# Optimization experiments

Hardware: AMD Instinct MI355X
Metric: run time of the kernel (lower is better)

## Reference

```python
import jax, jax.numpy as jnp
import numpy as np

N = 100000      # nodes
E = 1600000     # edges
P = 262144      # pos/neg candidate edges
IN = 128        # in_channels
HID = 64        # hidden_channels
HEADS = 2
NEG_SLOPE = 0.2  # PyG GATConv default


def setup_inputs() -> dict:
    key = jax.random.key(0)
    ks = jax.random.split(key, 16)
    g = lambda k, shape, fan_in: jax.random.normal(k, shape, jnp.float32) * (1.0 / np.sqrt(fan_in))
    return {
        "x": jax.random.normal(ks[0], (N, IN), jnp.float32),
        "edge_index": jax.random.randint(ks[1], (2, E), 0, N),
        "edge_weight": jax.random.uniform(ks[2], (E,), jnp.float32),
        "pos_edge_index": jax.random.randint(ks[3], (2, P), 0, N),
        "neg_edge_index": jax.random.randint(ks[4], (2, P), 0, N),
        # conv1: in -> HEADS*HID
        "W1": g(ks[5], (IN, HEADS * HID), IN),
        "att_src1": g(ks[6], (HEADS, HID), HID),
        "att_dst1": g(ks[7], (HEADS, HID), HID),
        "b1": jnp.zeros((HEADS * HID,), jnp.float32),
        # conv2: HEADS*HID -> HID (heads=1)
        "W2": g(ks[8], (HEADS * HID, HID), HEADS * HID),
        "att_src2": g(ks[9], (1, HID), HID),
        "att_dst2": g(ks[10], (1, HID), HID),
        "b2": jnp.zeros((HID,), jnp.float32),
        # link_pred: Linear(2*HID, 1)
        "link_W": g(ks[11], (2 * HID, 1), 2 * HID),
        "link_b": jnp.zeros((1,), jnp.float32),
    }


def gat_layer(x, src, dst, W, a_src, a_dst, bias, heads, out_c, concat):
    n = x.shape[0]
    xw = (x @ W).reshape(n, heads, out_c)                      # [N, H, C]
    alpha_src = jnp.sum(xw * a_src, axis=-1)                   # [N, H]
    alpha_dst = jnp.sum(xw * a_dst, axis=-1)                   # [N, H]
    e = jax.nn.leaky_relu(alpha_src[src] + alpha_dst[dst], NEG_SLOPE)  # [E, H]
    # segment softmax over edges grouped by destination node
    m = jax.ops.segment_max(e, dst, num_segments=n)            # [N, H]
    ex = jnp.exp(e - m[dst])
    s = jax.ops.segment_sum(ex, dst, num_segments=n)
    alpha = ex / s[dst]                                        # [E, H]
    out = jax.ops.segment_sum(xw[src] * alpha[..., None], dst, num_segments=n)  # [N, H, C]
    out = out.reshape(n, heads * out_c) if concat else out.mean(axis=1)
    return out + bias


def reference(x, edge_index, edge_weight, pos_edge_index, neg_edge_index,
              W1, att_src1, att_dst1, b1, W2, att_src2, att_dst2, b2,
              link_W, link_b):
    n = x.shape[0]
    # PyG GATConv add_self_loops=True
    loop = jnp.arange(n)
    src = jnp.concatenate([edge_index[0], loop])
    dst = jnp.concatenate([edge_index[1], loop])

    h = gat_layer(x, src, dst, W1, att_src1, att_dst1, b1, HEADS, HID, True)
    h = jax.nn.relu(h)
    z = gat_layer(h, src, dst, W2, att_src2, att_dst2, b2, 1, HID, True)

    def decode(ei):
        feat = jnp.concatenate([z[ei[0]], z[ei[1]]], axis=1)   # [P, 2*HID]
        return (feat @ link_W + link_b).squeeze(-1)

    return decode(pos_edge_index), decode(neg_edge_index)
```

## Files before the change

kernel.cpp:

```cpp
#include <hip/hip_runtime.h>

#define N_NODES 100000
#define E_EDGES 1600000
#define EP      (E_EDGES + N_NODES)
#define P_CAND  262144
#define IN_C    128
#define HID     64
#define NEG_SLOPE 0.2f

#define NBIN  196
#define NB2   256
#define EPB   ((EP + NB2 - 1) / NB2)
#define NTOT  (NBIN * NB2)

typedef _Float16 half4v __attribute__((ext_vector_type(4)));
typedef _Float16 half8v __attribute__((ext_vector_type(8)));
typedef float    float4v __attribute__((ext_vector_type(4)));


__global__ __launch_bounds__(256) void hist_kernel(const int* __restrict__ ei,
                                                   int* __restrict__ hist) {
    __shared__ int lh[NBIN];
    for (int t = threadIdx.x; t < NBIN; t += 256) lh[t] = 0;
    __syncthreads();
    int start = blockIdx.x * EPB;
    int end = min(start + EPB, EP);
    for (int i = start + threadIdx.x; i < end; i += 256) {
        int dst = (i < E_EDGES) ? ei[E_EDGES + i] : (i - E_EDGES);
        atomicAdd(&lh[dst >> 9], 1);
    }
    __syncthreads();
    for (int t = threadIdx.x; t < NBIN; t += 256) hist[t * NB2 + blockIdx.x] = lh[t];
}

__global__ __launch_bounds__(256) void scanA_kernel(const int* __restrict__ hist,
                                                    int* __restrict__ rowscan,
                                                    int* __restrict__ binsum) {
    int t = blockIdx.x;
    int c = threadIdx.x;
    int v = hist[t * NB2 + c];
    int lane = c & 63, w = c >> 6;
    int iv = v;
#pragma unroll
    for (int d = 1; d < 64; d <<= 1) {
        int o = __shfl_up(iv, d);
        if (lane >= d) iv += o;
    }
    __shared__ int wt[4];
    if (lane == 63) wt[w] = iv;
    __syncthreads();
    int add = 0;
    for (int i = 0; i < w; i++) add += wt[i];
    int inc = iv + add;
    rowscan[t * NB2 + c] = inc - v;
    if (c == 255) binsum[t] = inc;
}

__global__ __launch_bounds__(256) void scanB_kernel(const int* __restrict__ binsum,
                                                    int* __restrict__ binoff) {
    __shared__ int s[256];
    int c = threadIdx.x;
    int v = (c < NBIN) ? binsum[c] : 0;
    s[c] = v;
    __syncthreads();
    for (int d = 1; d < 256; d <<= 1) {
        int o = (c >= d) ? s[c - d] : 0;
        __syncthreads();
        s[c] += o;
        __syncthreads();
    }
    if (c == 0) binoff[0] = 0;
    if (c < NBIN) binoff[c + 1] = s[c];
}

__global__ __launch_bounds__(256) void scatterbin_kernel(const int* __restrict__ ei,
                                                         const int* __restrict__ rowscan,
                                                         const int* __restrict__ binoff,
                                                         unsigned* __restrict__ binned) {
    __shared__ int cur[NBIN];
    for (int t = threadIdx.x; t < NBIN; t += 256)
        cur[t] = binoff[t] + rowscan[t * NB2 + blockIdx.x];
    __syncthreads();
    int start = blockIdx.x * EPB;
    int end = min(start + EPB, EP);
    for (int i = start + threadIdx.x; i < end; i += 256) {
        int src, dst;
        if (i < E_EDGES) { src = ei[i]; dst = ei[E_EDGES + i]; }
        else             { src = i - E_EDGES; dst = src; }
        int pos = atomicAdd(&cur[dst >> 9], 1);
        binned[pos] = (unsigned)src | ((unsigned)(dst & 511) << 17);
    }
}

__global__ __launch_bounds__(1024) void binsort_kernel(const unsigned* __restrict__ binned,
                                                       const int* __restrict__ binoff,
                                                       int* __restrict__ off,
                                                       int* __restrict__ csr) {
    __shared__ int lh[512];
    __shared__ int wpre[8];
    int b = blockIdx.x, t = threadIdx.x;
    int base = binoff[b];
    int endv = binoff[b + 1];
    if (t < 512) lh[t] = 0;
    __syncthreads();
    for (int i = base + t; i < endv; i += 1024)
        atomicAdd(&lh[binned[i] >> 17], 1);
    __syncthreads();
    int iv = 0, lane = t & 63, w = t >> 6;
    if (t < 512) {
        iv = lh[t];
#pragma unroll
        for (int d = 1; d < 64; d <<= 1) {
            int o = __shfl_up(iv, d);
            if (lane >= d) iv += o;
        }
        if (lane == 63) wpre[w] = iv;
    }
    __syncthreads();
    if (t == 0) {
        int run = 0;
        for (int i = 0; i < 8; i++) { int x = wpre[i]; wpre[i] = run; run += x; }
    }
    __syncthreads();
    if (t < 512) {
        int ex = iv + wpre[w] - lh[t];
        int node = b * 512 + t;
        if (node <= N_NODES) off[node] = base + ex;
        lh[t] = base + ex;
    }
    __syncthreads();
    for (int i = base + t; i < endv; i += 1024) {
        unsigned v = binned[i];
        int pos = atomicAdd(&lh[v >> 17], 1);
        csr[pos] = (int)(v & 0x1FFFFu);
    }
}


__global__ __launch_bounds__(256) void prep_kernel(
        const float* __restrict__ W1, const float* __restrict__ W2,
        const float* __restrict__ att_src1, const float* __restrict__ att_dst1,
        const float* __restrict__ att_src2, const float* __restrict__ att_dst2,
        const float* __restrict__ b2, const float* __restrict__ lw,
        _Float16* __restrict__ W1T, _Float16* __restrict__ W2T,
        float* __restrict__ cvec) {
    int idx = blockIdx.x * 256 + threadIdx.x;
    if (idx < 16384) {
        int col = idx >> 7, k = idx & 127;
        W1T[idx] = (_Float16)W1[k * 128 + col];
    } else if (idx < 16896) {
        int j = idx - 16384;
        int c4 = j >> 7, k = j & 127;
        const float* av = (c4 < 2 ? att_src1 : att_dst1) + (c4 & 1) * 64;
        const float* wr = W1 + k * 128 + (c4 & 1) * 64;
        float s = 0.f;
        for (int c = 0; c < 64; c++) s += wr[c] * av[c];
        W1T[(128 + c4) * 128 + k] = (_Float16)s;
    } else if (idx < 18432) {
        W1T[132 * 128 + (idx - 16896)] = (_Float16)0.f;
    } else if (idx < 18944) {
        int j = idx - 18432;
        int c4 = j >> 7, k = j & 127;
        const float* av = (c4 == 0) ? att_src2 : (c4 == 1) ? att_dst2
                        : (c4 == 2) ? lw : (lw + 64);
        const float* wr = W2 + k * 64;
        float s = 0.f;
        for (int c = 0; c < 64; c++) s += wr[c] * av[c];
        W2T[c4 * 128 + k] = (_Float16)s;
    } else if (idx < 18946) {
        int c = idx - 18944;
        const float* lwp = lw + c * 64;
        float s = 0.f;
        for (int i = 0; i < 64; i++) s += b2[i] * lwp[i];
        cvec[c] = s;
    }
}


__global__ __launch_bounds__(256) void gemm1_kernel(
        const float* __restrict__ x, const _Float16* __restrict__ W1T,
        unsigned char* __restrict__ xw1q, float* __restrict__ asp1,
        float* __restrict__ ad1) {
    __shared__ _Float16 xs[64 * 136];
    int tid = threadIdx.x;
    int base = blockIdx.x * 64;
    int w = tid >> 6, l = tid & 63;
    int quad = l >> 4, lq = l & 15;
    int row = base + 16 * w + lq;
    size_t rb = (size_t)(row < N_NODES ? row : 0) * 32;
    const float4* x4 = (const float4*)x;
    float4 af[8];
#pragma unroll
    for (int ks = 0; ks < 4; ks++) {
        af[2 * ks]     = x4[rb + ks * 8 + quad * 2];
        af[2 * ks + 1] = x4[rb + ks * 8 + quad * 2 + 1];
    }
    half8v a[4];
#pragma unroll
    for (int ks = 0; ks < 4; ks++) {
        float4 u0 = af[2 * ks], u1 = af[2 * ks + 1];
        half8v t;
        t[0] = (_Float16)u0.x; t[1] = (_Float16)u0.y; t[2] = (_Float16)u0.z; t[3] = (_Float16)u0.w;
        t[4] = (_Float16)u1.x; t[5] = (_Float16)u1.y; t[6] = (_Float16)u1.z; t[7] = (_Float16)u1.w;
        a[ks] = t;
    }
    float4v acc[9];
#pragma unroll
    for (int t = 0; t < 9; t++) acc[t] = (float4v)0.f;
#pragma unroll
    for (int ks = 0; ks < 4; ++ks) {
#pragma unroll
        for (int t = 0; t < 9; t++) {
            half8v b = *(const half8v*)&W1T[(t * 16 + lq) * 128 + ks * 32 + quad * 8];
            acc[t] = __builtin_amdgcn_mfma_f32_16x16x32_f16(a[ks], b, acc[t], 0, 0, 0);
        }
    }
    if (lq < 4) {
#pragma unroll
        for (int r = 0; r < 4; r++) {
            int n = base + 16 * w + quad * 4 + r;
            if (n < N_NODES) {
                if (lq < 2) asp1[4 * n + lq] = acc[8][r];
                else        ad1[2 * n + (lq & 1)] = acc[8][r];
            }
        }
    }
#pragma unroll
    for (int t = 0; t < 8; t++)
#pragma unroll
        for (int r = 0; r < 4; r++)
            xs[(16 * w + quad * 4 + r) * 136 + t * 16 + lq] = (_Float16)acc[t][r];
    __syncthreads();
    int node = tid >> 2, seg = tid & 3;
    if (base + node < N_NODES) {
        float vals[32];
        float mx = 0.f;
#pragma unroll
        for (int i = 0; i < 4; i++) {
            half8v vv = *(const half8v*)&xs[node * 136 + seg * 32 + i * 8];
#pragma unroll
            for (int k = 0; k < 8; k++) {
                float f = (float)vv[k];
                vals[i * 8 + k] = f;
                mx = fmaxf(mx, fabsf(f));
            }
        }
        mx = fmaxf(mx, __shfl_xor(mx, 1));
        mx = fmaxf(mx, __shfl_xor(mx, 2));
        mx = fmaxf(mx, 1e-20f);
        float r = 127.f / mx;
        unsigned pk[8];
#pragma unroll
        for (int d = 0; d < 8; d++) {
            unsigned u0 = (unsigned)(__float2int_rn(vals[d * 4 + 0] * r) + 128);
            unsigned u1 = (unsigned)(__float2int_rn(vals[d * 4 + 1] * r) + 128);
            unsigned u2 = (unsigned)(__float2int_rn(vals[d * 4 + 2] * r) + 128);
            unsigned u3 = (unsigned)(__float2int_rn(vals[d * 4 + 3] * r) + 128);
            pk[d] = u0 | (u1 << 8) | (u2 << 16) | (u3 << 24);
        }
        unsigned* dst = (unsigned*)&xw1q[(size_t)(base + node) * 128 + seg * 32];
        *(uint4*)dst       = make_uint4(pk[0], pk[1], pk[2], pk[3]);
        *(uint4*)(dst + 4) = make_uint4(pk[4], pk[5], pk[6], pk[7]);
        if (seg == 0) asp1[4 * (base + node) + 2] = mx * (1.f / 127.f);
    }
}


__global__ __launch_bounds__(256) void agg1_kernel(
        const int* __restrict__ off, const int* __restrict__ csr_src,
        const float* __restrict__ asp1, const float* __restrict__ ad1,
        const unsigned char* __restrict__ xw1q, const float* __restrict__ b1,
        const _Float16* __restrict__ W2T, float* __restrict__ asp2) {
    __shared__ float2 esm[4][64];
    int wv = threadIdx.x >> 6, lane = threadIdx.x & 63;
    int ql = lane & 15;
    int gb = lane & 48;
    int n = blockIdx.x * 16 + (wv << 2) + (lane >> 4);
    int s = off[n], e = off[n + 1];
    float2 ad = *(const float2*)&ad1[2 * n];
    float adn0 = ad.x, adn1 = ad.y;
    const char* fl = (const char*)&esm[wv][gb] + ((ql >= 8) ? 4 : 0);
    const unsigned char* xq = xw1q + 8 * ql;
    float acc[8];
#pragma unroll
    for (int i = 0; i < 8; i++) acc[i] = 0.f;
    float sl0 = 0.f, sl1 = 0.f;
    float csum = 0.f;

#define DEQ1(QV, G) { \
    acc[0] = fmaf((float)((QV).x & 0xffu), (G), acc[0]); \
    acc[1] = fmaf((float)(((QV).x >> 8) & 0xffu), (G), acc[1]); \
    acc[2] = fmaf((float)(((QV).x >> 16) & 0xffu), (G), acc[2]); \
    acc[3] = fmaf((float)((QV).x >> 24), (G), acc[3]); \
    acc[4] = fmaf((float)((QV).y & 0xffu), (G), acc[4]); \
    acc[5] = fmaf((float)(((QV).y >> 8) & 0xffu), (G), acc[5]); \
    acc[6] = fmaf((float)(((QV).y >> 16) & 0xffu), (G), acc[6]); \
    acc[7] = fmaf((float)((QV).y >> 24), (G), acc[7]); }

    for (int b = s; b < e; b += 16) {
        int cnt = min(16, e - b);
        int l = ql < cnt ? ql : cnt - 1;
        int srcv = csr_src[b + l];
        float4 ap = *(const float4*)&asp1[4 * srcv];
        float e0 = ap.x + adn0; e0 = e0 > 0.f ? e0 : NEG_SLOPE * e0;
        float e1 = ap.y + adn1; e1 = e1 > 0.f ? e1 : NEG_SLOPE * e1;
        float f0v = (ql < cnt) ? __expf(e0) : 0.f;
        float f1v = (ql < cnt) ? __expf(e1) : 0.f;
        sl0 += f0v; sl1 += f1v;
        esm[wv][lane] = make_float2(f0v * ap.z, f1v * ap.z);
        int sj = __shfl(srcv, gb);
        uint2 qcur = *(const uint2*)&xq[(size_t)sj * 128];
        int j = 0;
        for (; j + 1 < cnt; ++j) {
            int sn = __shfl(srcv, gb + j + 1);
            uint2 qnxt = *(const uint2*)&xq[(size_t)sn * 128];
            float g = *(const float*)(fl + (size_t)j * 8);
            csum += g;
            DEQ1(qcur, g)
            qcur = qnxt;
        }
        { float g = *(const float*)(fl + (size_t)j * 8);
          csum += g; DEQ1(qcur, g) }
    }
#undef DEQ1
#pragma unroll
    for (int m = 8; m >= 1; m >>= 1) { sl0 += __shfl_xor(sl0, m); sl1 += __shfl_xor(sl1, m); }
    float sum = (ql >= 8) ? sl1 : sl0;
    float rs = __builtin_amdgcn_rcpf(sum);
    float base8 = -128.f * csum;
    int c = 8 * ql;
    float z[8];
#pragma unroll
    for (int i = 0; i < 8; i++) {
        float vv = fmaf(acc[i] + base8, rs, b1[c + i]);
        z[i] = vv > 0.f ? vv : 0.f;
    }
    half8v w0 = *(const half8v*)&W2T[0 * 128 + c];
    half8v w1 = *(const half8v*)&W2T[1 * 128 + c];
    half8v w2 = *(const half8v*)&W2T[2 * 128 + c];
    half8v w3 = *(const half8v*)&W2T[3 * 128 + c];
    float d0 = 0.f, d1 = 0.f, d2 = 0.f, d3 = 0.f;
#pragma unroll
    for (int i = 0; i < 8; i++) {
        d0 = fmaf(z[i], (float)w0[i], d0);
        d1 = fmaf(z[i], (float)w1[i], d1);
        d2 = fmaf(z[i], (float)w2[i], d2);
        d3 = fmaf(z[i], (float)w3[i], d3);
    }
#pragma unroll
    for (int m = 8; m >= 1; m >>= 1) {
        d0 += __shfl_xor(d0, m);
        d1 += __shfl_xor(d1, m);
        d2 += __shfl_xor(d2, m);
        d3 += __shfl_xor(d3, m);
    }
    if (ql == 0) {
        *(float4*)&asp2[4 * n] = make_float4(d0, d2, d3, d1);
    }
}


__global__ __launch_bounds__(256) void agg2_kernel(
        const int* __restrict__ off, const int* __restrict__ csr_src,
        const float* __restrict__ asp2, const float* __restrict__ cvec,
        float* __restrict__ u, float* __restrict__ v) {
    int wv = threadIdx.x >> 6, lane = threadIdx.x & 63;
    int ql = lane & 15;
    int n = blockIdx.x * 16 + (wv << 2) + (lane >> 4);
    int s = off[n], e = off[n + 1];
    float adn = asp2[4 * n + 3];
    float sf = 0.f, s1 = 0.f, s2 = 0.f;
    for (int j = s + ql; j < e; j += 16) {
        int srcv = csr_src[j];
        float4 ap = *(const float4*)&asp2[4 * srcv];
        float ev = ap.x + adn; ev = ev > 0.f ? ev : NEG_SLOPE * ev;
        float f = __expf(ev);
        sf += f;
        s1 = fmaf(f, ap.y, s1);
        s2 = fmaf(f, ap.z, s2);
    }
#pragma unroll
    for (int m = 8; m >= 1; m >>= 1) {
        sf += __shfl_xor(sf, m);
        s1 += __shfl_xor(s1, m);
        s2 += __shfl_xor(s2, m);
    }
    if (ql == 0) {
        float rs = __builtin_amdgcn_rcpf(sf);
        u[n] = fmaf(s1, rs, cvec[0]);
        v[n] = fmaf(s2, rs, cvec[1]);
    }
}


__global__ __launch_bounds__(256) void decode_kernel(
        const int* __restrict__ pos_ei, const int* __restrict__ neg_ei,
        const float* __restrict__ u, const float* __restrict__ v,
        const float* __restrict__ lb, float* __restrict__ out) {
    int idx = blockIdx.x * 256 + threadIdx.x;
    if (idx >= 2 * P_CAND) return;
    const int* ei; int p;
    if (idx < P_CAND) { ei = pos_ei; p = idx; }
    else              { ei = neg_ei; p = idx - P_CAND; }
    int sN = ei[p], dN = ei[P_CAND + p];
    out[idx] = u[sN] + v[dN] + lb[0];
}


extern "C" void kernel_launch(void* const* d_in, const int* in_sizes, int n_in,
                              void* d_out, int out_size, void* d_ws, size_t ws_size,
                              hipStream_t stream) {
    const float* x        = (const float*)d_in[0];
    const int*   ei       = (const int*)d_in[1];
    const int*   pos_ei   = (const int*)d_in[3];
    const int*   neg_ei   = (const int*)d_in[4];
    const float* W1       = (const float*)d_in[5];
    const float* att_src1 = (const float*)d_in[6];
    const float* att_dst1 = (const float*)d_in[7];
    const float* b1       = (const float*)d_in[8];
    const float* W2       = (const float*)d_in[9];
    const float* att_src2 = (const float*)d_in[10];
    const float* att_dst2 = (const float*)d_in[11];
    const float* b2       = (const float*)d_in[12];
    const float* lw       = (const float*)d_in[13];
    const float* lb       = (const float*)d_in[14];
    float* out = (float*)d_out;

    char* ws = (char*)d_ws;
    size_t o = 0;
    auto alloc = [&](size_t bytes) -> char* {
        char* p = ws + o;
        o += (bytes + 511) & ~(size_t)511;
        return p;
    };
    unsigned char* xw1q = (unsigned char*)alloc((size_t)N_NODES * 128);
    float*    asp1  = (float*)alloc((size_t)N_NODES * 4 * 4);
    float*    ad1   = (float*)alloc((size_t)N_NODES * 2 * 4);
    float*    asp2  = (float*)alloc((size_t)N_NODES * 4 * 4);
    float*    cvec  = (float*)alloc(512);
    float*    u     = (float*)alloc((size_t)N_NODES * 4);
    float*    v     = (float*)alloc((size_t)N_NODES * 4);
    int*      off   = (int*)alloc((size_t)(N_NODES + 1) * 4);
    int*      hist  = (int*)alloc((size_t)NTOT * 4);
    int*      rowscan = (int*)alloc((size_t)NTOT * 4);
    int*      binsum  = (int*)alloc(256 * 4);
    int*      binoff  = (int*)alloc(256 * 4);
    unsigned* binned= (unsigned*)alloc((size_t)EP * 4);
    int*      csr   = (int*)alloc((size_t)EP * 4);
    _Float16* W1T   = (_Float16*)alloc((size_t)144 * 128 * 2);
    _Float16* W2T   = (_Float16*)alloc((size_t)4 * 128 * 2);

    prep_kernel<<<75, 256, 0, stream>>>(W1, W2, att_src1, att_dst1, att_src2, att_dst2,
                                        b2, lw, W1T, W2T, cvec);
    hist_kernel<<<NB2, 256, 0, stream>>>(ei, hist);
    scanA_kernel<<<NBIN, 256, 0, stream>>>(hist, rowscan, binsum);
    scanB_kernel<<<1, 256, 0, stream>>>(binsum, binoff);
    scatterbin_kernel<<<NB2, 256, 0, stream>>>(ei, rowscan, binoff, binned);
    binsort_kernel<<<NBIN, 1024, 0, stream>>>(binned, binoff, off, csr);
    gemm1_kernel<<<(N_NODES + 63) / 64, 256, 0, stream>>>(x, W1T, xw1q, asp1, ad1);
    agg1_kernel<<<N_NODES / 16, 256, 0, stream>>>(off, csr, asp1, ad1, xw1q, b1, W2T, asp2);
    agg2_kernel<<<N_NODES / 16, 256, 0, stream>>>(off, csr, asp2, cvec, u, v);
    decode_kernel<<<(2 * P_CAND + 255) / 256, 256, 0, stream>>>(pos_ei, neg_ei, u, v, lb, out);
}
```

Baseline: 263.1 us.

## Merge preprocessing kernels to cut launches and overlap scatter with GEMM

```diff
diff --git a/kernel.cpp b/kernel.cpp
--- a/kernel.cpp
+++ b/kernel.cpp
@@ -12,30 +12,76 @@
 #define NB2   256
 #define EPB   ((EP + NB2 - 1) / NB2)
 #define NTOT  (NBIN * NB2)
+#define PREPB 75
 
 typedef _Float16 half4v __attribute__((ext_vector_type(4)));
 typedef _Float16 half8v __attribute__((ext_vector_type(8)));
 typedef float    float4v __attribute__((ext_vector_type(4)));
 
 
-__global__ __launch_bounds__(256) void hist_kernel(const int* __restrict__ ei,
-                                                   int* __restrict__ hist) {
+__global__ __launch_bounds__(256) void prep_hist_kernel(
+        const float* __restrict__ W1, const float* __restrict__ W2,
+        const float* __restrict__ att_src1, const float* __restrict__ att_dst1,
+        const float* __restrict__ att_src2, const float* __restrict__ att_dst2,
+        const float* __restrict__ b2, const float* __restrict__ lw,
+        _Float16* __restrict__ W1T, _Float16* __restrict__ W2T,
+        float* __restrict__ cvec,
+        const int* __restrict__ ei, int* __restrict__ hist,
+        int* __restrict__ cnt) {
+    if (blockIdx.x < PREPB) {
+        int idx = blockIdx.x * 256 + threadIdx.x;
+        if (idx == 0) *cnt = 0;
+        if (idx < 16384) {
+            int col = idx >> 7, k = idx & 127;
+            W1T[idx] = (_Float16)W1[k * 128 + col];
+        } else if (idx < 16896) {
+            int j = idx - 16384;
+            int c4 = j >> 7, k = j & 127;
+            const float* av = (c4 < 2 ? att_src1 : att_dst1) + (c4 & 1) * 64;
+            const float* wr = W1 + k * 128 + (c4 & 1) * 64;
+            float s = 0.f;
+            for (int c = 0; c < 64; c++) s += wr[c] * av[c];
+            W1T[(128 + c4) * 128 + k] = (_Float16)s;
+        } else if (idx < 18432) {
+            W1T[132 * 128 + (idx - 16896)] = (_Float16)0.f;
+        } else if (idx < 18944) {
+            int j = idx - 18432;
+            int c4 = j >> 7, k = j & 127;
+            const float* av = (c4 == 0) ? att_src2 : (c4 == 1) ? att_dst2
+                            : (c4 == 2) ? lw : (lw + 64);
+            const float* wr = W2 + k * 64;
+            float s = 0.f;
+            for (int c = 0; c < 64; c++) s += wr[c] * av[c];
+            W2T[c4 * 128 + k] = (_Float16)s;
+        } else if (idx < 18946) {
+            int c = idx - 18944;
+            const float* lwp = lw + c * 64;
+            float s = 0.f;
+            for (int i = 0; i < 64; i++) s += b2[i] * lwp[i];
+            cvec[c] = s;
+        }
+        return;
+    }
     __shared__ int lh[NBIN];
+    int hb = blockIdx.x - PREPB;
     for (int t = threadIdx.x; t < NBIN; t += 256) lh[t] = 0;
     __syncthreads();
-    int start = blockIdx.x * EPB;
+    int start = hb * EPB;
     int end = min(start + EPB, EP);
     for (int i = start + threadIdx.x; i < end; i += 256) {
         int dst = (i < E_EDGES) ? ei[E_EDGES + i] : (i - E_EDGES);
         atomicAdd(&lh[dst >> 9], 1);
     }
     __syncthreads();
-    for (int t = threadIdx.x; t < NBIN; t += 256) hist[t * NB2 + blockIdx.x] = lh[t];
-}
-
-__global__ __launch_bounds__(256) void scanA_kernel(const int* __restrict__ hist,
-                                                    int* __restrict__ rowscan,
-                                                    int* __restrict__ binsum) {
+    for (int t = threadIdx.x; t < NBIN; t += 256) hist[t * NB2 + hb] = lh[t];
+}
+
+
+__global__ __launch_bounds__(256) void scan_kernel(const int* __restrict__ hist,
+                                                   int* __restrict__ rowscan,
+                                                   int* __restrict__ binsum,
+                                                   int* __restrict__ binoff,
+                                                   int* __restrict__ cnt) {
     int t = blockIdx.x;
     int c = threadIdx.x;
     int v = hist[t * NB2 + c];
@@ -47,6 +93,7 @@
         if (lane >= d) iv += o;
     }
     __shared__ int wt[4];
+    __shared__ int isLast;
     if (lane == 63) wt[w] = iv;
     __syncthreads();
     int add = 0;
@@ -54,14 +101,15 @@
     int inc = iv + add;
     rowscan[t * NB2 + c] = inc - v;
     if (c == 255) binsum[t] = inc;
-}
-
-__global__ __launch_bounds__(256) void scanB_kernel(const int* __restrict__ binsum,
-                                                    int* __restrict__ binoff) {
+    __threadfence();
+    __syncthreads();
+    if (c == 0) isLast = (atomicAdd(cnt, 1) == NBIN - 1);
+    __syncthreads();
+    if (!isLast) return;
+    __threadfence();
     __shared__ int s[256];
-    int c = threadIdx.x;
-    int v = (c < NBIN) ? binsum[c] : 0;
-    s[c] = v;
+    int bv = (c < NBIN) ? binsum[c] : 0;
+    s[c] = bv;
     __syncthreads();
     for (int d = 1; d < 256; d <<= 1) {
         int o = (c >= d) ? s[c - d] : 0;
@@ -73,24 +121,114 @@
     if (c < NBIN) binoff[c + 1] = s[c];
 }
 
-__global__ __launch_bounds__(256) void scatterbin_kernel(const int* __restrict__ ei,
-                                                         const int* __restrict__ rowscan,
-                                                         const int* __restrict__ binoff,
-                                                         unsigned* __restrict__ binned) {
-    __shared__ int cur[NBIN];
-    for (int t = threadIdx.x; t < NBIN; t += 256)
-        cur[t] = binoff[t] + rowscan[t * NB2 + blockIdx.x];
-    __syncthreads();
-    int start = blockIdx.x * EPB;
-    int end = min(start + EPB, EP);
-    for (int i = start + threadIdx.x; i < end; i += 256) {
-        int src, dst;
-        if (i < E_EDGES) { src = ei[i]; dst = ei[E_EDGES + i]; }
-        else             { src = i - E_EDGES; dst = src; }
-        int pos = atomicAdd(&cur[dst >> 9], 1);
-        binned[pos] = (unsigned)src | ((unsigned)(dst & 511) << 17);
-    }
-}
+
+__global__ __launch_bounds__(256) void scatter_gemm_kernel(
+        const int* __restrict__ ei, const int* __restrict__ rowscan,
+        const int* __restrict__ binoff, unsigned* __restrict__ binned,
+        const float* __restrict__ x, const _Float16* __restrict__ W1T,
+        unsigned char* __restrict__ xw1q, float* __restrict__ asp1,
+        float* __restrict__ ad1) {
+    __shared__ __align__(16) char smem[64 * 136 * 2];
+    if (blockIdx.x < NB2) {
+        int* cur = (int*)smem;
+        for (int t = threadIdx.x; t < NBIN; t += 256)
+            cur[t] = binoff[t] + rowscan[t * NB2 + blockIdx.x];
+        __syncthreads();
+        int start = blockIdx.x * EPB;
+        int end = min(start + EPB, EP);
+        for (int i = start + threadIdx.x; i < end; i += 256) {
+            int src, dst;
+            if (i < E_EDGES) { src = ei[i]; dst = ei[E_EDGES + i]; }
+            else             { src = i - E_EDGES; dst = src; }
+            int pos = atomicAdd(&cur[dst >> 9], 1);
+            binned[pos] = (unsigned)src | ((unsigned)(dst & 511) << 17);
+        }
+        return;
+    }
+    _Float16* xs = (_Float16*)smem;
+    int tid = threadIdx.x;
+    int base = (blockIdx.x - NB2) * 64;
+    int w = tid >> 6, l = tid & 63;
+    int quad = l >> 4, lq = l & 15;
+    int row = base + 16 * w + lq;
+    size_t rb = (size_t)(row < N_NODES ? row : 0) * 32;
+    const float4* x4 = (const float4*)x;
+    float4 af[8];
+#pragma unroll
+    for (int ks = 0; ks < 4; ks++) {
+        af[2 * ks]     = x4[rb + ks * 8 + quad * 2];
+        af[2 * ks + 1] = x4[rb + ks * 8 + quad * 2 + 1];
+    }
+    half8v a[4];
+#pragma unroll
+    for (int ks = 0; ks < 4; ks++) {
+        float4 u0 = af[2 * ks], u1 = af[2 * ks + 1];
+        half8v t;
+        t[0] = (_Float16)u0.x; t[1] = (_Float16)u0.y; t[2] = (_Float16)u0.z; t[3] = (_Float16)u0.w;
+        t[4] = (_Float16)u1.x; t[5] = (_Float16)u1.y; t[6] = (_Float16)u1.z; t[7] = (_Float16)u1.w;
+        a[ks] = t;
+    }
+    float4v acc[9];
+#pragma unroll
+    for (int t = 0; t < 9; t++) acc[t] = (float4v)0.f;
+#pragma unroll
+    for (int ks = 0; ks < 4; ++ks) {
+#pragma unroll
+        for (int t = 0; t < 9; t++) {
+            half8v b = *(const half8v*)&W1T[(t * 16 + lq) * 128 + ks * 32 + quad * 8];
+            acc[t] = __builtin_amdgcn_mfma_f32_16x16x32_f16(a[ks], b, acc[t], 0, 0, 0);
+        }
+    }
+    if (lq < 4) {
+#pragma unroll
+        for (int r = 0; r < 4; r++) {
+            int n = base + 16 * w + quad * 4 + r;
+            if (n < N_NODES) {
+                if (lq < 2) asp1[4 * n + lq] = acc[8][r];
+                else        ad1[2 * n + (lq & 1)] = acc[8][r];
+            }
+        }
+    }
+#pragma unroll
+    for (int t = 0; t < 8; t++)
+#pragma unroll
+        for (int r = 0; r < 4; r++)
+            xs[(16 * w + quad * 4 + r) * 136 + t * 16 + lq] = (_Float16)acc[t][r];
+    __syncthreads();
+    int node = tid >> 2, seg = tid & 3;
+    if (base + node < N_NODES) {
+        float vals[32];
+        float mx = 0.f;
+#pragma unroll
+        for (int i = 0; i < 4; i++) {
+            half8v vv = *(const half8v*)&xs[node * 136 + seg * 32 + i * 8];
+#pragma unroll
+            for (int k = 0; k < 8; k++) {
+                float f = (float)vv[k];
+                vals[i * 8 + k] = f;
+                mx = fmaxf(mx, fabsf(f));
+            }
+        }
+        mx = fmaxf(mx, __shfl_xor(mx, 1));
+        mx = fmaxf(mx, __shfl_xor(mx, 2));
+        mx = fmaxf(mx, 1e-20f);
+        float r = 127.f / mx;
+        unsigned pk[8];
+#pragma unroll
+        for (int d = 0; d < 8; d++) {
+            unsigned u0 = (unsigned)(__float2int_rn(vals[d * 4 + 0] * r) + 128);
+            unsigned u1 = (unsigned)(__float2int_rn(vals[d * 4 + 1] * r) + 128);
+            unsigned u2 = (unsigned)(__float2int_rn(vals[d * 4 + 2] * r) + 128);
+            unsigned u3 = (unsigned)(__float2int_rn(vals[d * 4 + 3] * r) + 128);
+            pk[d] = u0 | (u1 << 8) | (u2 << 16) | (u3 << 24);
+        }
+        unsigned* dst = (unsigned*)&xw1q[(size_t)(base + node) * 128 + seg * 32];
+        *(uint4*)dst       = make_uint4(pk[0], pk[1], pk[2], pk[3]);
+        *(uint4*)(dst + 4) = make_uint4(pk[4], pk[5], pk[6], pk[7]);
+        if (seg == 0) asp1[4 * (base + node) + 2] = mx * (1.f / 127.f);
+    }
+}
+
 
 __global__ __launch_bounds__(1024) void binsort_kernel(const unsigned* __restrict__ binned,
                                                        const int* __restrict__ binoff,
@@ -133,135 +271,6 @@
         unsigned v = binned[i];
         int pos = atomicAdd(&lh[v >> 17], 1);
         csr[pos] = (int)(v & 0x1FFFFu);
-    }
-}
-
-
-__global__ __launch_bounds__(256) void prep_kernel(
-        const float* __restrict__ W1, const float* __restrict__ W2,
-        const float* __restrict__ att_src1, const float* __restrict__ att_dst1,
-        const float* __restrict__ att_src2, const float* __restrict__ att_dst2,
-        const float* __restrict__ b2, const float* __restrict__ lw,
-        _Float16* __restrict__ W1T, _Float16* __restrict__ W2T,
-        float* __restrict__ cvec) {
-    int idx = blockIdx.x * 256 + threadIdx.x;
-    if (idx < 16384) {
-        int col = idx >> 7, k = idx & 127;
-        W1T[idx] = (_Float16)W1[k * 128 + col];
-    } else if (idx < 16896) {
-        int j = idx - 16384;
-        int c4 = j >> 7, k = j & 127;
-        const float* av = (c4 < 2 ? att_src1 : att_dst1) + (c4 & 1) * 64;
-        const float* wr = W1 + k * 128 + (c4 & 1) * 64;
-        float s = 0.f;
-        for (int c = 0; c < 64; c++) s += wr[c] * av[c];
-        W1T[(128 + c4) * 128 + k] = (_Float16)s;
-    } else if (idx < 18432) {
-        W1T[132 * 128 + (idx - 16896)] = (_Float16)0.f;
-    } else if (idx < 18944) {
-        int j = idx - 18432;
-        int c4 = j >> 7, k = j & 127;
-        const float* av = (c4 == 0) ? att_src2 : (c4 == 1) ? att_dst2
-                        : (c4 == 2) ? lw : (lw + 64);
-        const float* wr = W2 + k * 64;
-        float s = 0.f;
-        for (int c = 0; c < 64; c++) s += wr[c] * av[c];
-        W2T[c4 * 128 + k] = (_Float16)s;
-    } else if (idx < 18946) {
-        int c = idx - 18944;
-        const float* lwp = lw + c * 64;
-        float s = 0.f;
-        for (int i = 0; i < 64; i++) s += b2[i] * lwp[i];
-        cvec[c] = s;
-    }
-}
-
-
-__global__ __launch_bounds__(256) void gemm1_kernel(
-        const float* __restrict__ x, const _Float16* __restrict__ W1T,
-        unsigned char* __restrict__ xw1q, float* __restrict__ asp1,
-        float* __restrict__ ad1) {
-    __shared__ _Float16 xs[64 * 136];
-    int tid = threadIdx.x;
-    int base = blockIdx.x * 64;
-    int w = tid >> 6, l = tid & 63;
-    int quad = l >> 4, lq = l & 15;
-    int row = base + 16 * w + lq;
-    size_t rb = (size_t)(row < N_NODES ? row : 0) * 32;
-    const float4* x4 = (const float4*)x;
-    float4 af[8];
-#pragma unroll
-    for (int ks = 0; ks < 4; ks++) {
-        af[2 * ks]     = x4[rb + ks * 8 + quad * 2];
-        af[2 * ks + 1] = x4[rb + ks * 8 + quad * 2 + 1];
-    }
-    half8v a[4];
-#pragma unroll
-    for (int ks = 0; ks < 4; ks++) {
-        float4 u0 = af[2 * ks], u1 = af[2 * ks + 1];
-        half8v t;
-        t[0] = (_Float16)u0.x; t[1] = (_Float16)u0.y; t[2] = (_Float16)u0.z; t[3] = (_Float16)u0.w;
-        t[4] = (_Float16)u1.x; t[5] = (_Float16)u1.y; t[6] = (_Float16)u1.z; t[7] = (_Float16)u1.w;
-        a[ks] = t;
-    }
-    float4v acc[9];
-#pragma unroll
-    for (int t = 0; t < 9; t++) acc[t] = (float4v)0.f;
-#pragma unroll
-    for (int ks = 0; ks < 4; ++ks) {
-#pragma unroll
-        for (int t = 0; t < 9; t++) {
-            half8v b = *(const half8v*)&W1T[(t * 16 + lq) * 128 + ks * 32 + quad * 8];
-            acc[t] = __builtin_amdgcn_mfma_f32_16x16x32_f16(a[ks], b, acc[t], 0, 0, 0);
-        }
-    }
-    if (lq < 4) {
-#pragma unroll
-        for (int r = 0; r < 4; r++) {
-            int n = base + 16 * w + quad * 4 + r;
-            if (n < N_NODES) {
-                if (lq < 2) asp1[4 * n + lq] = acc[8][r];
-                else        ad1[2 * n + (lq & 1)] = acc[8][r];
-            }
-        }
-    }
-#pragma unroll
-    for (int t = 0; t < 8; t++)
-#pragma unroll
-        for (int r = 0; r < 4; r++)
-            xs[(16 * w + quad * 4 + r) * 136 + t * 16 + lq] = (_Float16)acc[t][r];
-    __syncthreads();
-    int node = tid >> 2, seg = tid & 3;
-    if (base + node < N_NODES) {
-        float vals[32];
-        float mx = 0.f;
-#pragma unroll
-        for (int i = 0; i < 4; i++) {
-            half8v vv = *(const half8v*)&xs[node * 136 + seg * 32 + i * 8];
-#pragma unroll
-            for (int k = 0; k < 8; k++) {
-                float f = (float)vv[k];
-                vals[i * 8 + k] = f;
-                mx = fmaxf(mx, fabsf(f));
-            }
-        }
-        mx = fmaxf(mx, __shfl_xor(mx, 1));
-        mx = fmaxf(mx, __shfl_xor(mx, 2));
-        mx = fmaxf(mx, 1e-20f);
-        float r = 127.f / mx;
-        unsigned pk[8];
-#pragma unroll
-        for (int d = 0; d < 8; d++) {
-            unsigned u0 = (unsigned)(__float2int_rn(vals[d * 4 + 0] * r) + 128);
-            unsigned u1 = (unsigned)(__float2int_rn(vals[d * 4 + 1] * r) + 128);
-            unsigned u2 = (unsigned)(__float2int_rn(vals[d * 4 + 2] * r) + 128);
-            unsigned u3 = (unsigned)(__float2int_rn(vals[d * 4 + 3] * r) + 128);
-            pk[d] = u0 | (u1 << 8) | (u2 << 16) | (u3 << 24);
-        }
-        unsigned* dst = (unsigned*)&xw1q[(size_t)(base + node) * 128 + seg * 32];
-        *(uint4*)dst       = make_uint4(pk[0], pk[1], pk[2], pk[3]);
-        *(uint4*)(dst + 4) = make_uint4(pk[4], pk[5], pk[6], pk[7]);
-        if (seg == 0) asp1[4 * (base + node) + 2] = mx * (1.f / 127.f);
     }
 }
 
@@ -445,19 +454,19 @@
     int*      rowscan = (int*)alloc((size_t)NTOT * 4);
     int*      binsum  = (int*)alloc(256 * 4);
     int*      binoff  = (int*)alloc(256 * 4);
+    int*      cnt     = (int*)alloc(64);
     unsigned* binned= (unsigned*)alloc((size_t)EP * 4);
     int*      csr   = (int*)alloc((size_t)EP * 4);
     _Float16* W1T   = (_Float16*)alloc((size_t)144 * 128 * 2);
     _Float16* W2T   = (_Float16*)alloc((size_t)4 * 128 * 2);
 
-    prep_kernel<<<75, 256, 0, stream>>>(W1, W2, att_src1, att_dst1, att_src2, att_dst2,
-                                        b2, lw, W1T, W2T, cvec);
-    hist_kernel<<<NB2, 256, 0, stream>>>(ei, hist);
-    scanA_kernel<<<NBIN, 256, 0, stream>>>(hist, rowscan, binsum);
-    scanB_kernel<<<1, 256, 0, stream>>>(binsum, binoff);
-    scatterbin_kernel<<<NB2, 256, 0, stream>>>(ei, rowscan, binoff, binned);
+    prep_hist_kernel<<<PREPB + NB2, 256, 0, stream>>>(
+        W1, W2, att_src1, att_dst1, att_src2, att_dst2, b2, lw,
+        W1T, W2T, cvec, ei, hist, cnt);
+    scan_kernel<<<NBIN, 256, 0, stream>>>(hist, rowscan, binsum, binoff, cnt);
+    scatter_gemm_kernel<<<NB2 + (N_NODES + 63) / 64, 256, 0, stream>>>(
+        ei, rowscan, binoff, binned, x, W1T, xw1q, asp1, ad1);
     binsort_kernel<<<NBIN, 1024, 0, stream>>>(binned, binoff, off, csr);
-    gemm1_kernel<<<(N_NODES + 63) / 64, 256, 0, stream>>>(x, W1T, xw1q, asp1, ad1);
     agg1_kernel<<<N_NODES / 16, 256, 0, stream>>>(off, csr, asp1, ad1, xw1q, b1, W2T, asp2);
     agg2_kernel<<<N_NODES / 16, 256, 0, stream>>>(off, csr, asp2, cvec, u, v);
     decode_kernel<<<(2 * P_CAND + 255) / 256, 256, 0, stream>>>(pos_ei, neg_ei, u, v, lb, out);
```

New measurement: 268.2 us. No clear change (+1.9%).

## Replace two-level bin sort CSR build with global atomic degree count and scatter

Applied to the files above, without the earlier changes.

```diff
diff --git a/kernel.cpp b/kernel.cpp
--- a/kernel.cpp
+++ b/kernel.cpp
@@ -11,130 +11,12 @@
 #define NBIN  196
 #define NB2   256
 #define EPB   ((EP + NB2 - 1) / NB2)
-#define NTOT  (NBIN * NB2)
+#define PREPB 75
+#define ZBLK  391
 
 typedef _Float16 half4v __attribute__((ext_vector_type(4)));
 typedef _Float16 half8v __attribute__((ext_vector_type(8)));
 typedef float    float4v __attribute__((ext_vector_type(4)));
-
-
-__global__ __launch_bounds__(256) void hist_kernel(const int* __restrict__ ei,
-                                                   int* __restrict__ hist) {
-    __shared__ int lh[NBIN];
-    for (int t = threadIdx.x; t < NBIN; t += 256) lh[t] = 0;
-    __syncthreads();
-    int start = blockIdx.x * EPB;
-    int end = min(start + EPB, EP);
-    for (int i = start + threadIdx.x; i < end; i += 256) {
-        int dst = (i < E_EDGES) ? ei[E_EDGES + i] : (i - E_EDGES);
-        atomicAdd(&lh[dst >> 9], 1);
-    }
-    __syncthreads();
-    for (int t = threadIdx.x; t < NBIN; t += 256) hist[t * NB2 + blockIdx.x] = lh[t];
-}
-
-__global__ __launch_bounds__(256) void scanA_kernel(const int* __restrict__ hist,
-                                                    int* __restrict__ rowscan,
-                                                    int* __restrict__ binsum) {
-    int t = blockIdx.x;
-    int c = threadIdx.x;
-    int v = hist[t * NB2 + c];
-    int lane = c & 63, w = c >> 6;
-    int iv = v;
-#pragma unroll
-    for (int d = 1; d < 64; d <<= 1) {
-        int o = __shfl_up(iv, d);
-        if (lane >= d) iv += o;
-    }
-    __shared__ int wt[4];
-    if (lane == 63) wt[w] = iv;
-    __syncthreads();
-    int add = 0;
-    for (int i = 0; i < w; i++) add += wt[i];
-    int inc = iv + add;
-    rowscan[t * NB2 + c] = inc - v;
-    if (c == 255) binsum[t] = inc;
-}
-
-__global__ __launch_bounds__(256) void scanB_kernel(const int* __restrict__ binsum,
-                                                    int* __restrict__ binoff) {
-    __shared__ int s[256];
-    int c = threadIdx.x;
-    int v = (c < NBIN) ? binsum[c] : 0;
-    s[c] = v;
-    __syncthreads();
-    for (int d = 1; d < 256; d <<= 1) {
-        int o = (c >= d) ? s[c - d] : 0;
-        __syncthreads();
-        s[c] += o;
-        __syncthreads();
-    }
-    if (c == 0) binoff[0] = 0;
-    if (c < NBIN) binoff[c + 1] = s[c];
-}
-
-__global__ __launch_bounds__(256) void scatterbin_kernel(const int* __restrict__ ei,
-                                                         const int* __restrict__ rowscan,
-                                                         const int* __restrict__ binoff,
-                                                         unsigned* __restrict__ binned) {
-    __shared__ int cur[NBIN];
-    for (int t = threadIdx.x; t < NBIN; t += 256)
-        cur[t] = binoff[t] + rowscan[t * NB2 + blockIdx.x];
-    __syncthreads();
-    int start = blockIdx.x * EPB;
-    int end = min(start + EPB, EP);
-    for (int i = start + threadIdx.x; i < end; i += 256) {
-        int src, dst;
-        if (i < E_EDGES) { src = ei[i]; dst = ei[E_EDGES + i]; }
-        else             { src = i - E_EDGES; dst = src; }
-        int pos = atomicAdd(&cur[dst >> 9], 1);
-        binned[pos] = (unsigned)src | ((unsigned)(dst & 511) << 17);
-    }
-}
-
-__global__ __launch_bounds__(1024) void binsort_kernel(const unsigned* __restrict__ binned,
-                                                       const int* __restrict__ binoff,
-                                                       int* __restrict__ off,
-                                                       int* __restrict__ csr) {
-    __shared__ int lh[512];
-    __shared__ int wpre[8];
-    int b = blockIdx.x, t = threadIdx.x;
-    int base = binoff[b];
-    int endv = binoff[b + 1];
-    if (t < 512) lh[t] = 0;
-    __syncthreads();
-    for (int i = base + t; i < endv; i += 1024)
-        atomicAdd(&lh[binned[i] >> 17], 1);
-    __syncthreads();
-    int iv = 0, lane = t & 63, w = t >> 6;
-    if (t < 512) {
-        iv = lh[t];
-#pragma unroll
-        for (int d = 1; d < 64; d <<= 1) {
-            int o = __shfl_up(iv, d);
-            if (lane >= d) iv += o;
-        }
-        if (lane == 63) wpre[w] = iv;
-    }
-    __syncthreads();
-    if (t == 0) {
-        int run = 0;
-        for (int i = 0; i < 8; i++) { int x = wpre[i]; wpre[i] = run; run += x; }
-    }
-    __syncthreads();
-    if (t < 512) {
-        int ex = iv + wpre[w] - lh[t];
-        int node = b * 512 + t;
-        if (node <= N_NODES) off[node] = base + ex;
-        lh[t] = base + ex;
-    }
-    __syncthreads();
-    for (int i = base + t; i < endv; i += 1024) {
-        unsigned v = binned[i];
-        int pos = atomicAdd(&lh[v >> 17], 1);
-        csr[pos] = (int)(v & 0x1FFFFu);
-    }
-}
 
 
 __global__ __launch_bounds__(256) void prep_kernel(
@@ -143,7 +25,12 @@
         const float* __restrict__ att_src2, const float* __restrict__ att_dst2,
         const float* __restrict__ b2, const float* __restrict__ lw,
         _Float16* __restrict__ W1T, _Float16* __restrict__ W2T,
-        float* __restrict__ cvec) {
+        float* __restrict__ cvec, int* __restrict__ deg) {
+    if (blockIdx.x >= PREPB) {
+        int z = (blockIdx.x - PREPB) * 256 + threadIdx.x;
+        if (z < N_NODES) deg[z] = 0;
+        return;
+    }
     int idx = blockIdx.x * 256 + threadIdx.x;
     if (idx < 16384) {
         int col = idx >> 7, k = idx & 127;
@@ -177,6 +64,99 @@
 }
 
 
+__global__ __launch_bounds__(256) void deghist_kernel(const int* __restrict__ ei,
+                                                      int* __restrict__ deg) {
+    int start = blockIdx.x * EPB;
+    int end = min(start + EPB, EP);
+    for (int i = start + threadIdx.x; i < end; i += 256) {
+        int dst = (i < E_EDGES) ? ei[E_EDGES + i] : (i - E_EDGES);
+        atomicAdd(&deg[dst], 1);
+    }
+}
+
+
+__global__ __launch_bounds__(512) void nodered_kernel(const int* __restrict__ deg,
+                                                      int* __restrict__ bsum) {
+    __shared__ int ws[8];
+    int b = blockIdx.x, t = threadIdx.x;
+    int node = b * 512 + t;
+    int d = (node < N_NODES) ? deg[node] : 0;
+    int lane = t & 63, w = t >> 6;
+    int r = d;
+#pragma unroll
+    for (int m = 32; m >= 1; m >>= 1) r += __shfl_xor(r, m);
+    if (lane == 0) ws[w] = r;
+    __syncthreads();
+    if (t == 0) {
+        int s = 0;
+        for (int i = 0; i < 8; i++) s += ws[i];
+        bsum[b] = s;
+    }
+}
+
+
+__global__ __launch_bounds__(256) void bscan_kernel(const int* __restrict__ bsum,
+                                                    int* __restrict__ boff) {
+    __shared__ int s[256];
+    int c = threadIdx.x;
+    int v = (c < NBIN) ? bsum[c] : 0;
+    s[c] = v;
+    __syncthreads();
+    for (int d = 1; d < 256; d <<= 1) {
+        int o = (c >= d) ? s[c - d] : 0;
+        __syncthreads();
+        s[c] += o;
+        __syncthreads();
+    }
+    if (c == 0) boff[0] = 0;
+    if (c < NBIN) boff[c + 1] = s[c];
+}
+
+
+__global__ __launch_bounds__(512) void nodescan_kernel(const int* __restrict__ deg,
+                                                       const int* __restrict__ boff,
+                                                       int* __restrict__ off,
+                                                       int* __restrict__ cur) {
+    __shared__ int wpre[8];
+    int b = blockIdx.x, t = threadIdx.x;
+    int node = b * 512 + t;
+    int d = (node < N_NODES) ? deg[node] : 0;
+    int lane = t & 63, w = t >> 6;
+    int iv = d;
+#pragma unroll
+    for (int m = 1; m < 64; m <<= 1) {
+        int o = __shfl_up(iv, m);
+        if (lane >= m) iv += o;
+    }
+    if (lane == 63) wpre[w] = iv;
+    __syncthreads();
+    if (t == 0) {
+        int run = 0;
+        for (int i = 0; i < 8; i++) { int x = wpre[i]; wpre[i] = run; run += x; }
+    }
+    __syncthreads();
+    int ex = iv + wpre[w] - d;
+    int pos = boff[b] + ex;
+    if (node <= N_NODES) off[node] = pos;
+    if (node < N_NODES) cur[node] = pos;
+}
+
+
+__global__ __launch_bounds__(256) void scatter_kernel(const int* __restrict__ ei,
+                                                      int* __restrict__ cur,
+                                                      int* __restrict__ csr) {
+    int start = blockIdx.x * EPB;
+    int end = min(start + EPB, EP);
+    for (int i = start + threadIdx.x; i < end; i += 256) {
+        int src, dst;
+        if (i < E_EDGES) { src = ei[i]; dst = ei[E_EDGES + i]; }
+        else             { src = i - E_EDGES; dst = src; }
+        int pos = atomicAdd(&cur[dst], 1);
+        csr[pos] = src;
+    }
+}
+
+
 __global__ __launch_bounds__(256) void gemm1_kernel(
         const float* __restrict__ x, const _Float16* __restrict__ W1T,
         unsigned char* __restrict__ xw1q, float* __restrict__ asp1,
@@ -440,23 +420,22 @@
     float*    cvec  = (float*)alloc(512);
     float*    u     = (float*)alloc((size_t)N_NODES * 4);
     float*    v     = (float*)alloc((size_t)N_NODES * 4);
+    int*      deg   = (int*)alloc((size_t)N_NODES * 4);
+    int*      cur   = (int*)alloc((size_t)N_NODES * 4);
     int*      off   = (int*)alloc((size_t)(N_NODES + 1) * 4);
-    int*      hist  = (int*)alloc((size_t)NTOT * 4);
-    int*      rowscan = (int*)alloc((size_t)NTOT * 4);
-    int*      binsum  = (int*)alloc(256 * 4);
-    int*      binoff  = (int*)alloc(256 * 4);
-    unsigned* binned= (unsigned*)alloc((size_t)EP * 4);
+    int*      bsum  = (int*)alloc(256 * 4);
+    int*      boff  = (int*)alloc(256 * 4);
     int*      csr   = (int*)alloc((size_t)EP * 4);
     _Float16* W1T   = (_Float16*)alloc((size_t)144 * 128 * 2);
     _Float16* W2T   = (_Float16*)alloc((size_t)4 * 128 * 2);
 
-    prep_kernel<<<75, 256, 0, stream>>>(W1, W2, att_src1, att_dst1, att_src2, att_dst2,
-                                        b2, lw, W1T, W2T, cvec);
-    hist_kernel<<<NB2, 256, 0, stream>>>(ei, hist);
-    scanA_kernel<<<NBIN, 256, 0, stream>>>(hist, rowscan, binsum);
-    scanB_kernel<<<1, 256, 0, stream>>>(binsum, binoff);
-    scatterbin_kernel<<<NB2, 256, 0, stream>>>(ei, rowscan, binoff, binned);
-    binsort_kernel<<<NBIN, 1024, 0, stream>>>(binned, binoff, off, csr);
+    prep_kernel<<<PREPB + ZBLK, 256, 0, stream>>>(
+        W1, W2, att_src1, att_dst1, att_src2, att_dst2, b2, lw, W1T, W2T, cvec, deg);
+    deghist_kernel<<<NB2, 256, 0, stream>>>(ei, deg);
+    nodered_kernel<<<NBIN, 512, 0, stream>>>(deg, bsum);
+    bscan_kernel<<<1, 256, 0, stream>>>(bsum, boff);
+    nodescan_kernel<<<NBIN, 512, 0, stream>>>(deg, boff, off, cur);
+    scatter_kernel<<<NB2, 256, 0, stream>>>(ei, cur, csr);
     gemm1_kernel<<<(N_NODES + 63) / 64, 256, 0, stream>>>(x, W1T, xw1q, asp1, ad1);
     agg1_kernel<<<N_NODES / 16, 256, 0, stream>>>(off, csr, asp1, ad1, xw1q, b1, W2T, asp2);
     agg2_kernel<<<N_NODES / 16, 256, 0, stream>>>(off, csr, asp2, cvec, u, v);
```

Result: slower. 425.8 us (+61.9%).
